# Performance work log

Hardware: AMD Instinct MI355X
Metric: run time of the kernel (lower is better)

## Reference

```python
import jax, jax.numpy as jnp
import numpy as np

N, K, F_IN, F_HID, F_OUT = 500000, 16, 7, 40, 3

def setup_inputs() -> dict:
    key = jax.random.key(0)
    k1, k2, k3 = jax.random.split(key, 3)
    mailbox = jax.random.normal(k1, (N, K, F_IN), dtype=jnp.float32)
    W1 = jax.random.normal(k2, (F_IN, F_HID), dtype=jnp.float32) * (1.0 / np.sqrt(F_IN))
    b1 = jnp.zeros((F_HID,), dtype=jnp.float32)
    W2 = jax.random.normal(k3, (F_HID, F_OUT), dtype=jnp.float32) * (1.0 / np.sqrt(F_HID))
    b2 = jnp.zeros((F_OUT,), dtype=jnp.float32)
    return {"mailbox": mailbox, "W1": W1, "b1": b1, "W2": W2, "b2": b2}

def reference(mailbox, W1, b1, W2, b2):
    # MLP 7->40->3 applied per (node, neighbor) message, then mean over neighbors.
    h = jax.nn.relu(jnp.einsum('nkf,fh->nkh', mailbox, W1) + b1)  # [N,K,40]
    y = jnp.einsum('nkh,ho->nko', h, W2) + b2                     # [N,K,3]
    return jnp.mean(y, axis=1)                                    # [N,3]
```

## Files before the change

### kernel.cpp

```cpp
#include <hip/hip_runtime.h>

#define N_NODES 500000
#define K_NB 16
#define F_IN 7
#define F_HID 40
#define F_OUT 3

__global__ __launch_bounds__(256) void aggre_kernel(
    const float* __restrict__ mailbox,
    const float* __restrict__ W1,
    const float* __restrict__ b1,
    const float* __restrict__ W2,
    const float* __restrict__ b2,
    float* __restrict__ out)
{
    __shared__ float4 w1lds[F_HID * 2];
    __shared__ float4 w2lds[F_HID];

    const int t = threadIdx.x;
    if (t < F_HID * 2) {
        const int h = t >> 1;
        float4 v;
        if ((t & 1) == 0) {
            v.x = W1[0 * F_HID + h]; v.y = W1[1 * F_HID + h];
            v.z = W1[2 * F_HID + h]; v.w = W1[3 * F_HID + h];
        } else {
            v.x = W1[4 * F_HID + h]; v.y = W1[5 * F_HID + h];
            v.z = W1[6 * F_HID + h]; v.w = b1[h];
        }
        w1lds[t] = v;
    } else if (t < F_HID * 2 + F_HID) {
        const int h = t - F_HID * 2;
        float4 v;
        v.x = W2[h * F_OUT + 0];
        v.y = W2[h * F_OUT + 1];
        v.z = W2[h * F_OUT + 2];
        v.w = 0.0f;
        w2lds[h] = v;
    }
    __syncthreads();

    const int n = blockIdx.x * blockDim.x + threadIdx.x;
    if (n >= N_NODES) return;

    float4 mb[28];
    const float4* __restrict__ src =
        (const float4*)(mailbox + (size_t)n * (K_NB * F_IN));
    #pragma unroll
    for (int i = 0; i < 28; ++i) mb[i] = src[i];
    const float* m = (const float*)mb;

    float a0 = 0.0f, a1 = 0.0f, a2 = 0.0f;

    for (int h = 0; h < F_HID; ++h) {
        const float4 wa = w1lds[h * 2 + 0];
        const float4 wb = w1lds[h * 2 + 1];
        float sh = 0.0f;
        #pragma unroll
        for (int k = 0; k < K_NB; ++k) {
            const float* mk = m + k * F_IN;
            float acc = wb.w;
            acc = fmaf(mk[0], wa.x, acc);
            acc = fmaf(mk[1], wa.y, acc);
            acc = fmaf(mk[2], wa.z, acc);
            acc = fmaf(mk[3], wa.w, acc);
            acc = fmaf(mk[4], wb.x, acc);
            acc = fmaf(mk[5], wb.y, acc);
            acc = fmaf(mk[6], wb.z, acc);
            sh += fmaxf(acc, 0.0f);
        }
        const float4 w2v = w2lds[h];
        a0 = fmaf(sh, w2v.x, a0);
        a1 = fmaf(sh, w2v.y, a1);
        a2 = fmaf(sh, w2v.z, a2);
    }

    const float inv = 1.0f / (float)K_NB;
    float* __restrict__ op = out + (size_t)n * F_OUT;
    op[0] = fmaf(a0, inv, b2[0]);
    op[1] = fmaf(a1, inv, b2[1]);
    op[2] = fmaf(a2, inv, b2[2]);
}

extern "C" void kernel_launch(void* const* d_in, const int* in_sizes, int n_in,
                              void* d_out, int out_size, void* d_ws, size_t ws_size,
                              hipStream_t stream) {
    const float* mailbox = (const float*)d_in[0];
    const float* W1      = (const float*)d_in[1];
    const float* b1      = (const float*)d_in[2];
    const float* W2      = (const float*)d_in[3];
    const float* b2      = (const float*)d_in[4];
    float* out = (float*)d_out;

    const int threads = 256;
    const int blocks = (N_NODES + threads - 1) / threads;
    aggre_kernel<<<blocks, threads, 0, stream>>>(mailbox, W1, b1, W2, b2, out);
}
```

Before: 325.6 us.

## Stage mailbox via direct global-to-LDS loads and split nodes across four lanes

Each wave now copies a contiguous tile of 16 nodes into LDS with the global_load_lds builtin, so the global reads are fully coalesced instead of each thread streaming 448 strided bytes. Four lanes then share each node, each handling 4 neighbors, and the partial sums are combined with xor shuffles. This cuts per-thread register pressure from 112 mailbox floats to 28 and should raise occupancy. It adds LDS traffic and shuffles, and it assumes N is a multiple of 16 nodes per wave because there is no per-node bounds check inside the tile.

```diff
diff --git a/kernel.cpp b/kernel.cpp
--- a/kernel.cpp
+++ b/kernel.cpp
@@ -1,10 +1,18 @@
 #include <hip/hip_runtime.h>
+#include <stdint.h>
 
 #define N_NODES 500000
 #define K_NB 16
 #define F_IN 7
 #define F_HID 40
 #define F_OUT 3
+#define NODE_FLOATS (K_NB * F_IN)
+#define NPW 16
+#define WPB 4
+#define NPB (NPW * WPB)
+
+typedef __attribute__((address_space(3))) void lds_void_t;
+typedef __attribute__((address_space(1))) const void glb_void_t;
 
 __global__ __launch_bounds__(256) void aggre_kernel(
     const float* __restrict__ mailbox,
@@ -16,6 +24,7 @@
 {
     __shared__ float4 w1lds[F_HID * 2];
     __shared__ float4 w2lds[F_HID];
+    __shared__ __align__(16) float tile[WPB][NPW * NODE_FLOATS];
 
     const int t = threadIdx.x;
     if (t < F_HID * 2) {
@@ -29,7 +38,7 @@
             v.z = W1[6 * F_HID + h]; v.w = b1[h];
         }
         w1lds[t] = v;
-    } else if (t < F_HID * 2 + F_HID) {
+    } else if (t < F_HID * 3) {
         const int h = t - F_HID * 2;
         float4 v;
         v.x = W2[h * F_OUT + 0];
@@ -40,33 +49,50 @@
     }
     __syncthreads();
 
-    const int n = blockIdx.x * blockDim.x + threadIdx.x;
-    if (n >= N_NODES) return;
+    const int wave = t >> 6;
+    const int lane = t & 63;
+    const long tile0 = (long)blockIdx.x * NPB + (long)wave * NPW;
+    if (tile0 >= N_NODES) return;
 
-    float4 mb[28];
-    const float4* __restrict__ src =
-        (const float4*)(mailbox + (size_t)n * (K_NB * F_IN));
+    const float* gsrc = mailbox + (size_t)tile0 * NODE_FLOATS;
     #pragma unroll
-    for (int i = 0; i < 28; ++i) mb[i] = src[i];
-    const float* m = (const float*)mb;
+    for (int j = 0; j < 7; ++j) {
+        const float* g = gsrc + (size_t)(j * 64 + lane) * 4;
+        __builtin_amdgcn_global_load_lds(
+            (glb_void_t*)g,
+            (lds_void_t*)&tile[wave][j * 256],
+            16, 0, 0);
+    }
+    __builtin_amdgcn_s_waitcnt(0x0f70);
+
+    const int nloc = lane >> 2;
+    const int r = lane & 3;
+    const float* mp = &tile[wave][nloc * NODE_FLOATS + r * 28];
+    float m[28];
+    #pragma unroll
+    for (int i = 0; i < 7; ++i) {
+        const float4 v = ((const float4*)mp)[i];
+        m[4 * i + 0] = v.x; m[4 * i + 1] = v.y;
+        m[4 * i + 2] = v.z; m[4 * i + 3] = v.w;
+    }
 
     float a0 = 0.0f, a1 = 0.0f, a2 = 0.0f;
-
+    #pragma unroll 2
     for (int h = 0; h < F_HID; ++h) {
-        const float4 wa = w1lds[h * 2 + 0];
-        const float4 wb = w1lds[h * 2 + 1];
+        const float4 wa = w1lds[2 * h + 0];
+        const float4 wb = w1lds[2 * h + 1];
         float sh = 0.0f;
         #pragma unroll
-        for (int k = 0; k < K_NB; ++k) {
-            const float* mk = m + k * F_IN;
+        for (int kk = 0; kk < 4; ++kk) {
+            const int o = kk * F_IN;
             float acc = wb.w;
-            acc = fmaf(mk[0], wa.x, acc);
-            acc = fmaf(mk[1], wa.y, acc);
-            acc = fmaf(mk[2], wa.z, acc);
-            acc = fmaf(mk[3], wa.w, acc);
-            acc = fmaf(mk[4], wb.x, acc);
-            acc = fmaf(mk[5], wb.y, acc);
-            acc = fmaf(mk[6], wb.z, acc);
+            acc = fmaf(m[o + 0], wa.x, acc);
+            acc = fmaf(m[o + 1], wa.y, acc);
+            acc = fmaf(m[o + 2], wa.z, acc);
+            acc = fmaf(m[o + 3], wa.w, acc);
+            acc = fmaf(m[o + 4], wb.x, acc);
+            acc = fmaf(m[o + 5], wb.y, acc);
+            acc = fmaf(m[o + 6], wb.z, acc);
             sh += fmaxf(acc, 0.0f);
         }
         const float4 w2v = w2lds[h];
@@ -75,11 +101,15 @@
         a2 = fmaf(sh, w2v.z, a2);
     }
 
-    const float inv = 1.0f / (float)K_NB;
-    float* __restrict__ op = out + (size_t)n * F_OUT;
-    op[0] = fmaf(a0, inv, b2[0]);
-    op[1] = fmaf(a1, inv, b2[1]);
-    op[2] = fmaf(a2, inv, b2[2]);
+    a0 += __shfl_xor(a0, 1); a0 += __shfl_xor(a0, 2);
+    a1 += __shfl_xor(a1, 1); a1 += __shfl_xor(a1, 2);
+    a2 += __shfl_xor(a2, 1); a2 += __shfl_xor(a2, 2);
+
+    if (r < F_OUT) {
+        const float val = (r == 0) ? a0 : ((r == 1) ? a1 : a2);
+        out[(size_t)(tile0 + nloc) * F_OUT + r] =
+            fmaf(val, 1.0f / (float)K_NB, b2[r]);
+    }
 }
 
 extern "C" void kernel_launch(void* const* d_in, const int* in_sizes, int n_in,
@@ -92,7 +122,6 @@
     const float* b2      = (const float*)d_in[4];
     float* out = (float*)d_out;
 
-    const int threads = 256;
-    const int blocks = (N_NODES + threads - 1) / threads;
-    aggre_kernel<<<blocks, threads, 0, stream>>>(mailbox, W1, b1, W2, b2, out);
+    const int blocks = (N_NODES + NPB - 1) / NPB;
+    aggre_kernel<<<blocks, 256, 0, stream>>>(mailbox, W1, b1, W2, b2, out);
 }
```

Result: faster. 315.4 us (-3.1%).
